# Kernel tuning notes

Measured on AMD Instinct MI355X. Metric: run time of the kernel, lower is better.

The kernel has to match this reference:

```python
import jax, jax.numpy as jnp
import numpy as np

B, C, F, H = 16384, 64, 128, 128  # batch, conv1d_out_channel, in_features, hidden


def setup_inputs() -> dict:
    key = jax.random.key(0)
    k_x, k_w1, k_w2 = jax.random.split(key, 3)
    inputline = jax.random.normal(k_x, (B, C, F), dtype=jnp.float32)
    # Per-channel cloned Flowconf MLP params: Linear(F,H) -> ReLU -> Linear(H,1)
    W1 = jax.random.normal(k_w1, (C, F, H), dtype=jnp.float32) * (1.0 / np.sqrt(F))
    b1 = jnp.zeros((C, H), dtype=jnp.float32)
    W2 = jax.random.normal(k_w2, (C, H), dtype=jnp.float32) * (1.0 / np.sqrt(H))
    b2 = jnp.zeros((C,), dtype=jnp.float32)
    return {"inputline": inputline, "W1": W1, "b1": b1, "W2": W2, "b2": b2}


def reference(inputline, W1, b1, W2, b2) -> jnp.ndarray:
    # Batched over channels: replaces the Python loop over C cloned submodules
    # with indexed assignment into output[:, i].
    h = jax.nn.relu(jnp.einsum("bcf,cfh->bch", inputline, W1) + b1)  # [B,C,H]
    out = jnp.einsum("bch,ch->bc", h, W2) + b2                        # [B,C]
    return out.sum(axis=-1)                                           # [B]
```

## Files before the change

kernel.cpp:

```cpp
#include <hip/hip_runtime.h>
#include <hip/hip_bf16.h>

#define B_TOT 16384
#define C_CH  64
#define F_IN  128
#define H_HID 128
#define CG    4
#define TROWS 32
#define NSUB  32
#define ROWS  (NSUB * TROWS)

using f32x4  = __attribute__((ext_vector_type(4))) float;
using bf16x8 = __attribute__((ext_vector_type(8))) short;

__device__ inline unsigned pack2(float a, float b) {
    unsigned short lo = __builtin_bit_cast(unsigned short, __float2bfloat16(a));
    unsigned short hi = __builtin_bit_cast(unsigned short, __float2bfloat16(b));
    return (unsigned)lo | ((unsigned)hi << 16);
}

__device__ inline void gld_lds16(const float* g, float* l) {
    __builtin_amdgcn_global_load_lds(
        (const __attribute__((address_space(1))) void*)g,
        (__attribute__((address_space(3))) void*)l, 16, 0, 0);
}

__device__ inline void issue_tile(const float* __restrict__ X, size_t base0,
                                  int wave, int lane, float* buf) {
    #pragma unroll
    for (int q = 0; q < 4; ++q) {
        const int r = wave * 4 + q;
        const float* rowp = X + base0 + (size_t)r * (C_CH * F_IN);
        const int sw = r & 7;
        #pragma unroll
        for (int h = 0; h < 2; ++h)
            gld_lds16(rowp + h * 256 + ((lane ^ sw) << 2),
                      buf + r * 512 + h * 256);
    }
}

__device__ inline float compute_group(const float* __restrict__ xb, int g,
                                      const bf16x8 (&wf)[4][4],
                                      const f32x4 (&w2c)[4],
                                      const f32x4 (&b1c)[4],
                                      int l15, int lg, int ch)
{
    f32x4 acc[4];
    #pragma unroll
    for (int nf = 0; nf < 4; ++nf) acc[nf] = b1c[nf];

    const int sw = l15 & 7;
    const int rb = (g * 16 + l15) * 512 + (ch >> 1) * 256;
    #pragma unroll
    for (int ks = 0; ks < 4; ++ks) {
        const int u = (ch & 1) * 32 + ks * 8 + lg * 2;
        float4 r0 = *reinterpret_cast<const float4*>(xb + rb + ((u ^ sw) << 2));
        float4 r1 = *reinterpret_cast<const float4*>(xb + rb + (((u + 1) ^ sw) << 2));
        uint4 px;
        px.x = pack2(r0.x, r0.y);
        px.y = pack2(r0.z, r0.w);
        px.z = pack2(r1.x, r1.y);
        px.w = pack2(r1.z, r1.w);
        bf16x8 xfrag = __builtin_bit_cast(bf16x8, px);
        #pragma unroll
        for (int nf = 0; nf < 4; ++nf)
            acc[nf] = __builtin_amdgcn_mfma_f32_16x16x32_bf16(
                wf[nf][ks], xfrag, acc[nf], 0, 0, 0);
    }

    float val = 0.f;
    #pragma unroll
    for (int nf = 0; nf < 4; ++nf)
        #pragma unroll
        for (int j = 0; j < 4; ++j)
            val += fmaxf(acc[nf][j], 0.f) * w2c[nf][j];
    val += __shfl_xor(val, 16, 64);
    val += __shfl_xor(val, 32, 64);
    return val;
}

__global__ __launch_bounds__(512, 2)
void fused_mlp_kernel(const float* __restrict__ X,
                      const float* __restrict__ W1,
                      const float* __restrict__ b1,
                      const float* __restrict__ W2,
                      const float* __restrict__ b2,
                      float* __restrict__ out)
{
    __shared__ alignas(16) float Xs[2 * TROWS * 512];

    const int t    = threadIdx.x;
    const int lane = t & 63;
    const int wave = t >> 6;
    const int l15  = lane & 15;
    const int lg   = lane >> 4;
    const int ch   = wave & 3;
    const int hh   = wave >> 2;

    const int c0 = blockIdx.x * CG;
    const int c  = c0 + ch;
    const int m0 = blockIdx.y * ROWS;

    float* bu0 = Xs;
    float* bu1 = Xs + TROWS * 512;

    const size_t cbase = ((size_t)m0 * C_CH + c0) * F_IN;
    const size_t tstep = (size_t)TROWS * C_CH * F_IN;
    issue_tile(X, cbase, wave, lane, bu0);
    issue_tile(X, cbase + tstep, wave, lane, bu1);

    bf16x8 wf[4][4];
    {
        const float* wb = W1 + (size_t)c * F_IN * H_HID + hh * 64 + l15;
        #pragma unroll
        for (int nf = 0; nf < 4; ++nf)
            #pragma unroll
            for (int ks = 0; ks < 4; ++ks) {
                const int f0 = ks * 32 + lg * 8;
                float v[8];
                #pragma unroll
                for (int e = 0; e < 8; ++e)
                    v[e] = wb[(size_t)(f0 + e) * H_HID + nf * 16];
                uint4 p;
                p.x = pack2(v[0], v[1]);
                p.y = pack2(v[2], v[3]);
                p.z = pack2(v[4], v[5]);
                p.w = pack2(v[6], v[7]);
                wf[nf][ks] = __builtin_bit_cast(bf16x8, p);
            }
    }
    f32x4 w2c[4], b1c[4];
    #pragma unroll
    for (int nf = 0; nf < 4; ++nf) {
        const int ho = c * H_HID + hh * 64 + nf * 16 + lg * 4;
        w2c[nf] = *reinterpret_cast<const f32x4*>(W2 + ho);
        b1c[nf] = *reinterpret_cast<const f32x4*>(b1 + ho);
    }
    const float b2c = (hh == 0) ? b2[c] : 0.f;

    #pragma unroll 1
    for (int sc = 0; sc < NSUB; ++sc) {
        asm volatile("s_waitcnt vmcnt(2)" ::: "memory");
        __builtin_amdgcn_s_barrier();
        asm volatile("" ::: "memory");

        const float* xb = (sc & 1) ? bu1 : bu0;
        float*       nb = (sc & 1) ? bu0 : bu1;
        if (sc + 1 < NSUB)
            issue_tile(X, cbase + (size_t)(sc + 1) * tstep, wave, lane, nb);

        float v0 = compute_group(xb, 0, wf, w2c, b1c, l15, lg, ch);
        if (lane < 16) atomicAdd(&out[m0 + sc * TROWS + lane], v0 + b2c);
        float v1 = compute_group(xb, 1, wf, w2c, b1c, l15, lg, ch);
        if (lane < 16) atomicAdd(&out[m0 + sc * TROWS + 16 + lane], v1 + b2c);
    }
}

extern "C" void kernel_launch(void* const* d_in, const int* in_sizes, int n_in,
                              void* d_out, int out_size, void* d_ws, size_t ws_size,
                              hipStream_t stream) {
    const float* X  = (const float*)d_in[0];
    const float* W1 = (const float*)d_in[1];
    const float* b1 = (const float*)d_in[2];
    const float* W2 = (const float*)d_in[3];
    const float* b2 = (const float*)d_in[4];
    float* out = (float*)d_out;

    hipMemsetAsync(out, 0, (size_t)out_size * sizeof(float), stream);

    dim3 grid(C_CH / CG, B_TOT / ROWS);
    fused_mlp_kernel<<<grid, dim3(512), 0, stream>>>(X, W1, b1, W2, b2, out);
}
```

Before: 108.6 us.

## Widen blocks to eight channels with sixteen-row tiles and LDS-resident W2/b1

Each block now covers 8 channels with 1024 threads and stages 16 batch rows per tile, so each wave loads one full row of the input tile. Each wave's 16 rows are now handled in a single MFMA pass instead of two. W2 and b1 slices move from per-lane registers into shared memory, and the bias add is deferred to the epilogue. The aim is to cut register pressure, get larger contiguous loads per row and keep the double-buffered prefetch. The launch-bounds hint of four 1024-thread blocks cannot be met in hardware and may force very tight register limits or spills, and the wait count was retuned for fewer loads per tile.

```diff
diff --git a/kernel.cpp b/kernel.cpp
--- a/kernel.cpp
+++ b/kernel.cpp
@@ -5,8 +5,8 @@
 #define C_CH  64
 #define F_IN  128
 #define H_HID 128
-#define CG    4
-#define TROWS 32
+#define CG    8
+#define TROWS 16
 #define NSUB  32
 #define ROWS  (NSUB * TROWS)
 
@@ -27,59 +27,15 @@
 
 __device__ inline void issue_tile(const float* __restrict__ X, size_t base0,
                                   int wave, int lane, float* buf) {
+    const float* rowp = X + base0 + (size_t)wave * (C_CH * F_IN);
+    const int sw = wave & 7;
+    float* dst = buf + wave * 1024;
     #pragma unroll
-    for (int q = 0; q < 4; ++q) {
-        const int r = wave * 4 + q;
-        const float* rowp = X + base0 + (size_t)r * (C_CH * F_IN);
-        const int sw = r & 7;
-        #pragma unroll
-        for (int h = 0; h < 2; ++h)
-            gld_lds16(rowp + h * 256 + ((lane ^ sw) << 2),
-                      buf + r * 512 + h * 256);
-    }
+    for (int h = 0; h < 4; ++h)
+        gld_lds16(rowp + h * 256 + ((lane ^ sw) << 2), dst + h * 256);
 }
 
-__device__ inline float compute_group(const float* __restrict__ xb, int g,
-                                      const bf16x8 (&wf)[4][4],
-                                      const f32x4 (&w2c)[4],
-                                      const f32x4 (&b1c)[4],
-                                      int l15, int lg, int ch)
-{
-    f32x4 acc[4];
-    #pragma unroll
-    for (int nf = 0; nf < 4; ++nf) acc[nf] = b1c[nf];
-
-    const int sw = l15 & 7;
-    const int rb = (g * 16 + l15) * 512 + (ch >> 1) * 256;
-    #pragma unroll
-    for (int ks = 0; ks < 4; ++ks) {
-        const int u = (ch & 1) * 32 + ks * 8 + lg * 2;
-        float4 r0 = *reinterpret_cast<const float4*>(xb + rb + ((u ^ sw) << 2));
-        float4 r1 = *reinterpret_cast<const float4*>(xb + rb + (((u + 1) ^ sw) << 2));
-        uint4 px;
-        px.x = pack2(r0.x, r0.y);
-        px.y = pack2(r0.z, r0.w);
-        px.z = pack2(r1.x, r1.y);
-        px.w = pack2(r1.z, r1.w);
-        bf16x8 xfrag = __builtin_bit_cast(bf16x8, px);
-        #pragma unroll
-        for (int nf = 0; nf < 4; ++nf)
-            acc[nf] = __builtin_amdgcn_mfma_f32_16x16x32_bf16(
-                wf[nf][ks], xfrag, acc[nf], 0, 0, 0);
-    }
-
-    float val = 0.f;
-    #pragma unroll
-    for (int nf = 0; nf < 4; ++nf)
-        #pragma unroll
-        for (int j = 0; j < 4; ++j)
-            val += fmaxf(acc[nf][j], 0.f) * w2c[nf][j];
-    val += __shfl_xor(val, 16, 64);
-    val += __shfl_xor(val, 32, 64);
-    return val;
-}
-
-__global__ __launch_bounds__(512, 2)
+__global__ __launch_bounds__(1024, 4)
 void fused_mlp_kernel(const float* __restrict__ X,
                       const float* __restrict__ W1,
                       const float* __restrict__ b1,
@@ -87,27 +43,32 @@
                       const float* __restrict__ b2,
                       float* __restrict__ out)
 {
-    __shared__ alignas(16) float Xs[2 * TROWS * 512];
+    __shared__ alignas(16) float Xs[2 * TROWS * 1024];
+    __shared__ alignas(16) float w2t[CG * H_HID];
+    __shared__ alignas(16) float b1t[CG * H_HID];
 
     const int t    = threadIdx.x;
     const int lane = t & 63;
     const int wave = t >> 6;
     const int l15  = lane & 15;
     const int lg   = lane >> 4;
-    const int ch   = wave & 3;
-    const int hh   = wave >> 2;
+    const int ch   = wave & 7;
+    const int hh   = wave >> 3;
 
     const int c0 = blockIdx.x * CG;
     const int c  = c0 + ch;
     const int m0 = blockIdx.y * ROWS;
 
     float* bu0 = Xs;
-    float* bu1 = Xs + TROWS * 512;
+    float* bu1 = Xs + TROWS * 1024;
 
     const size_t cbase = ((size_t)m0 * C_CH + c0) * F_IN;
     const size_t tstep = (size_t)TROWS * C_CH * F_IN;
     issue_tile(X, cbase, wave, lane, bu0);
     issue_tile(X, cbase + tstep, wave, lane, bu1);
+
+    w2t[t] = W2[c0 * H_HID + t];
+    b1t[t] = b1[c0 * H_HID + t];
 
     bf16x8 wf[4][4];
     {
@@ -129,18 +90,11 @@
                 wf[nf][ks] = __builtin_bit_cast(bf16x8, p);
             }
     }
-    f32x4 w2c[4], b1c[4];
-    #pragma unroll
-    for (int nf = 0; nf < 4; ++nf) {
-        const int ho = c * H_HID + hh * 64 + nf * 16 + lg * 4;
-        w2c[nf] = *reinterpret_cast<const f32x4*>(W2 + ho);
-        b1c[nf] = *reinterpret_cast<const f32x4*>(b1 + ho);
-    }
     const float b2c = (hh == 0) ? b2[c] : 0.f;
 
     #pragma unroll 1
     for (int sc = 0; sc < NSUB; ++sc) {
-        asm volatile("s_waitcnt vmcnt(2)" ::: "memory");
+        asm volatile("s_waitcnt vmcnt(1)" ::: "memory");
         __builtin_amdgcn_s_barrier();
         asm volatile("" ::: "memory");
 
@@ -149,10 +103,42 @@
         if (sc + 1 < NSUB)
             issue_tile(X, cbase + (size_t)(sc + 1) * tstep, wave, lane, nb);
 
-        float v0 = compute_group(xb, 0, wf, w2c, b1c, l15, lg, ch);
-        if (lane < 16) atomicAdd(&out[m0 + sc * TROWS + lane], v0 + b2c);
-        float v1 = compute_group(xb, 1, wf, w2c, b1c, l15, lg, ch);
-        if (lane < 16) atomicAdd(&out[m0 + sc * TROWS + 16 + lane], v1 + b2c);
+        f32x4 acc[4];
+        #pragma unroll
+        for (int nf = 0; nf < 4; ++nf) acc[nf] = f32x4{0.f, 0.f, 0.f, 0.f};
+
+        const int sw = l15 & 7;
+        const int rb = l15 * 1024 + (ch >> 1) * 256;
+        #pragma unroll
+        for (int ks = 0; ks < 4; ++ks) {
+            const int u = (ch & 1) * 32 + ks * 8 + lg * 2;
+            float4 r0 = *reinterpret_cast<const float4*>(xb + rb + ((u ^ sw) << 2));
+            float4 r1 = *reinterpret_cast<const float4*>(xb + rb + (((u + 1) ^ sw) << 2));
+            uint4 px;
+            px.x = pack2(r0.x, r0.y);
+            px.y = pack2(r0.z, r0.w);
+            px.z = pack2(r1.x, r1.y);
+            px.w = pack2(r1.z, r1.w);
+            bf16x8 xfrag = __builtin_bit_cast(bf16x8, px);
+            #pragma unroll
+            for (int nf = 0; nf < 4; ++nf)
+                acc[nf] = __builtin_amdgcn_mfma_f32_16x16x32_bf16(
+                    wf[nf][ks], xfrag, acc[nf], 0, 0, 0);
+        }
+
+        float val = 0.f;
+        #pragma unroll
+        for (int nf = 0; nf < 4; ++nf) {
+            const int ho = ch * H_HID + hh * 64 + nf * 16 + lg * 4;
+            f32x4 w2c = *reinterpret_cast<const f32x4*>(&w2t[ho]);
+            f32x4 b1c = *reinterpret_cast<const f32x4*>(&b1t[ho]);
+            #pragma unroll
+            for (int j = 0; j < 4; ++j)
+                val += fmaxf(acc[nf][j] + b1c[j], 0.f) * w2c[j];
+        }
+        val += __shfl_xor(val, 16, 64);
+        val += __shfl_xor(val, 32, 64);
+        if (lane < 16) atomicAdd(&out[m0 + sc * TROWS + lane], val + b2c);
     }
 }
 
@@ -169,5 +155,5 @@
     hipMemsetAsync(out, 0, (size_t)out_size * sizeof(float), stream);
 
     dim3 grid(C_CH / CG, B_TOT / ROWS);
-    fused_mlp_kernel<<<grid, dim3(512), 0, stream>>>(X, W1, b1, W2, b2, out);
+    fused_mlp_kernel<<<grid, dim3(1024), 0, stream>>>(X, W1, b1, W2, b2, out);
 }
```

New measurement: 121.4 us. 11.8% more time.
